# Optimization experiments

Hardware: AMD Instinct MI355X
Metric: run time of the kernel (lower is better)

Reference implementation:

```python
import jax, jax.numpy as jnp
import numpy as np

EPS = 1e-08  # matches torch default eps in both F.normalize and PairwiseDistance


def setup_inputs() -> dict:
    key = jax.random.key(0)
    x = jax.random.normal(key, (8192, 1024), dtype=jnp.float32)
    return {"x": x}


def reference(x) -> jnp.ndarray:
    B = x.shape[0]
    # F.normalize(x, p=2, dim=-1, eps=EPS): x / max(||x||_2, eps)
    norms = jnp.linalg.norm(x, axis=-1, keepdims=True)
    xn = x / jnp.maximum(norms, EPS)
    # cosine similarity matrix [B, B]
    cos_sim = xn @ xn.T
    # fill_diagonal_(-2): exclude self from nearest-neighbor search
    idx = jnp.arange(B)
    cos_sim = cos_sim.at[idx, idx].set(-2.0)
    nn_idx = jnp.argmax(cos_sim, axis=1)  # [B] int
    # torch PairwiseDistance(p=2, eps=EPS): ||x1 - x2 + eps||_2
    diff = xn - xn[nn_idx] + EPS
    nn_dist = jnp.sqrt(jnp.sum(diff * diff, axis=-1))  # [B]
    loss = -jnp.mean(jnp.log(nn_dist + EPS))
    return loss
```

## Files before the change

### kernel.cpp

```cpp
#include <hip/hip_runtime.h>
#include <hip/hip_bf16.h>
#include <math.h>

#define NB 8192
#define ND 1024
#define KEPS 1e-8f
#define SLOTS 128
#define NTILE 32
#define NWG 528
#define NKT 16

typedef __attribute__((ext_vector_type(8))) __bf16 bf16x8;
typedef __attribute__((ext_vector_type(4))) float f32x4;

__device__ __forceinline__ unsigned int fmono(float f) {
    unsigned int b = __float_as_uint(f);
    return b ^ ((b & 0x80000000u) ? 0xFFFFFFFFu : 0x80000000u);
}
__device__ __forceinline__ unsigned short f2bf(float f) {
    union { float f; unsigned int u; } a;
    a.f = f;
    unsigned int lsb = (a.u >> 16) & 1u;
    a.u += 0x7fffu + lsb;
    return (unsigned short)(a.u >> 16);
}
__device__ __forceinline__ void gload_lds16(const void* g, void* l) {
    __builtin_amdgcn_global_load_lds(
        (const __attribute__((address_space(1))) unsigned int*)g,
        (__attribute__((address_space(3))) unsigned int*)l, 16, 0, 0);
}
__device__ __forceinline__ unsigned long long packmax(float mx, int mc) {
    return ((unsigned long long)fmono(mx) << 32) |
           (unsigned long long)(~(unsigned int)mc);
}

__global__ __launch_bounds__(256) void normalize_k(const float* __restrict__ x,
                                                   unsigned short* __restrict__ xnb) {
    int row = blockIdx.x * 4 + (threadIdx.x >> 6);
    int l = threadIdx.x & 63;
    const float4* xr = (const float4*)(x + (size_t)row * ND);
    float4 v[4];
    float ss = 0.f;
#pragma unroll
    for (int q = 0; q < 4; ++q) {
        v[q] = xr[q * 64 + l];
        ss += v[q].x * v[q].x + v[q].y * v[q].y + v[q].z * v[q].z + v[q].w * v[q].w;
    }
#pragma unroll
    for (int off = 1; off < 64; off <<= 1) ss += __shfl_xor(ss, off, 64);
    float scale = 1.0f / fmaxf(sqrtf(ss), KEPS);
    ushort4* o = (ushort4*)(xnb + (size_t)row * ND);
#pragma unroll
    for (int q = 0; q < 4; ++q) {
        ushort4 u;
        u.x = f2bf(v[q].x * scale);
        u.y = f2bf(v[q].y * scale);
        u.z = f2bf(v[q].z * scale);
        u.w = f2bf(v[q].w * scale);
        o[q * 64 + l] = u;
    }
}

#define FENCE_BARRIER() do { asm volatile("" ::: "memory"); \
    __builtin_amdgcn_s_barrier(); asm volatile("" ::: "memory"); } while (0)
#define WAIT_VM6() asm volatile("s_waitcnt vmcnt(6)" ::: "memory")
#define WAIT_VM0() asm volatile("s_waitcnt vmcnt(0)" ::: "memory")

#define STAGE(H, DB) do { \
    gload_lds16(sp[H][0], ldsb + (DB) + (H) * 16384 + wv * 1024); \
    gload_lds16(sp[H][1], ldsb + (DB) + (H) * 16384 + 8192 + wv * 1024); \
    sp[H][0] += 128; sp[H][1] += 128; } while (0)

#define LOAD_A(CB, MQ) do { \
    const char* Ab_ = ldsb + (CB) + ((MQ) * 2 + wM) * 8192 + rowOff; \
    _Pragma("unroll") for (int mi = 0; mi < 4; ++mi) { \
        af[mi][0] = *(const bf16x8*)(Ab_ + mi * 2048 + ks0); \
        af[mi][1] = *(const bf16x8*)(Ab_ + mi * 2048 + ks1); } } while (0)

#define LOAD_B(CB, BANK, NQ) do { \
    const char* Bb_ = ldsb + (CB) + 32768 + (NQ) * 16384 + wN * 4096 + rowOff; \
    _Pragma("unroll") for (int ni = 0; ni < 2; ++ni) { \
        BANK[ni][0] = *(const bf16x8*)(Bb_ + ni * 2048 + ks0); \
        BANK[ni][1] = *(const bf16x8*)(Bb_ + ni * 2048 + ks1); } } while (0)

#define MFMAQ(MH, NH, BANK) do { \
    __builtin_amdgcn_s_setprio(1); \
    _Pragma("unroll") for (int mi = 0; mi < 4; ++mi) \
    _Pragma("unroll") for (int ni = 0; ni < 2; ++ni) { \
        acc[(MH) * 4 + mi][(NH) * 2 + ni] = __builtin_amdgcn_mfma_f32_16x16x32_bf16( \
            af[mi][0], BANK[ni][0], acc[(MH) * 4 + mi][(NH) * 2 + ni], 0, 0, 0); \
        acc[(MH) * 4 + mi][(NH) * 2 + ni] = __builtin_amdgcn_mfma_f32_16x16x32_bf16( \
            af[mi][1], BANK[ni][1], acc[(MH) * 4 + mi][(NH) * 2 + ni], 0, 0, 0); } \
    __builtin_amdgcn_s_setprio(0); } while (0)

#define KTILE(CB, DB, S1, S2, FINAL) do { \
    bf16x8 af[4][2], b0[2][2], b1[2][2]; \
    LOAD_A(CB, 0); LOAD_B(CB, b0, 0); \
    if (S1) STAGE(1, DB); \
    FENCE_BARRIER(); MFMAQ(0, 0, b0); FENCE_BARRIER(); \
    LOAD_B(CB, b1, 1); \
    if (S2) STAGE(0, CB); \
    FENCE_BARRIER(); MFMAQ(0, 1, b1); FENCE_BARRIER(); \
    LOAD_A(CB, 1); \
    if (S2) STAGE(2, CB); \
    FENCE_BARRIER(); MFMAQ(1, 1, b1); FENCE_BARRIER(); \
    if (S2) STAGE(3, CB); \
    MFMAQ(1, 0, b0); \
    if (FINAL) { WAIT_VM0(); } else { WAIT_VM6(); } \
    FENCE_BARRIER(); } while (0)

#define KTILE_LAST(CB) do { \
    bf16x8 af[4][2], b0[2][2], b1[2][2]; \
    LOAD_A(CB, 0); LOAD_B(CB, b0, 0); \
    FENCE_BARRIER(); MFMAQ(0, 0, b0); FENCE_BARRIER(); \
    LOAD_B(CB, b1, 1); \
    FENCE_BARRIER(); MFMAQ(0, 1, b1); FENCE_BARRIER(); \
    LOAD_A(CB, 1); \
    FENCE_BARRIER(); MFMAQ(1, 1, b1); FENCE_BARRIER(); \
    MFMAQ(1, 0, b0); } while (0)

__global__ __launch_bounds__(512, 2) void argmax_gemm(const unsigned short* __restrict__ xnb,
                                                      unsigned long long* __restrict__ partial) {
    extern __shared__ char ldsb[];

    int wg = (int)blockIdx.x;
    int tile = (wg & 7) * (NWG / 8) + (wg >> 3);
    int by = 0, tr = tile;
    while (tr >= NTILE - by) { tr -= NTILE - by; ++by; }
    const int bx = by + tr;

    const int rowBase = by * 256, colBase = bx * 256;
    const int tid = (int)threadIdx.x;
    const int wv = tid >> 6;
    const int l = tid & 63;
    const int wM = wv >> 2;
    const int wN = wv & 3;

    const int rowOff = (l & 15) * 128;
    const int ks0 = (((l >> 4) * 16)) ^ ((l & 7) << 4);
    const int ks1 = (64 | ((l >> 4) * 16)) ^ ((l & 7) << 4);

    const int scol = (((l & 7) ^ (l >> 3)) << 4);
    const char* xb = (const char*)xnb;
    const char* sp[4][2];
#pragma unroll
    for (int q = 0; q < 2; ++q) {
        int R = (q * 8 + wv) * 8 + (l >> 3);
        int arow = (R >> 6) * 128 + (R & 63);
        int bcol = (R >> 5) * 64 + (R & 31);
        sp[0][q] = xb + (size_t)(rowBase + arow) * 2048 + scol;
        sp[1][q] = xb + (size_t)(rowBase + arow + 64) * 2048 + scol;
        sp[2][q] = xb + (size_t)(colBase + bcol) * 2048 + scol;
        sp[3][q] = xb + (size_t)(colBase + bcol + 32) * 2048 + scol;
    }

    STAGE(0, 0); STAGE(2, 0); STAGE(3, 0); STAGE(1, 0);
    STAGE(0, 65536); STAGE(2, 65536); STAGE(3, 65536);

    f32x4 acc[8][4];
#pragma unroll
    for (int m = 0; m < 8; ++m)
#pragma unroll
        for (int n = 0; n < 4; ++n) acc[m][n] = f32x4{0.f, 0.f, 0.f, 0.f};

    WAIT_VM6();
    FENCE_BARRIER();

    for (int c = 0; c < 12; c += 2) {
        KTILE(0, 65536, true, true, false);
        KTILE(65536, 0, true, true, false);
    }
    KTILE(0, 65536, true, true, false);
    KTILE(65536, 0, true, true, false);
    KTILE(0, 65536, true, false, true);
    KTILE_LAST(65536);

#pragma unroll
    for (int m = 0; m < 8; ++m) {
#pragma unroll
        for (int r = 0; r < 4; ++r) {
            int gi = rowBase + wM * 128 + m * 16 + (l >> 4) * 4 + r;
            float mx = -3.0f;
            int mc = 0x7FFFFFFF;
#pragma unroll
            for (int n = 0; n < 4; ++n) {
                int gj = colBase + wN * 64 + n * 16 + (l & 15);
                float v = (gi == gj) ? -2.0f : acc[m][n][r];
                if (v > mx) { mx = v; mc = gj; }
            }
#pragma unroll
            for (int off = 1; off < 16; off <<= 1) {
                float omx = __shfl_xor(mx, off, 64);
                int omc = __shfl_xor(mc, off, 64);
                if (omx > mx || (omx == mx && omc < mc)) { mx = omx; mc = omc; }
            }
            if ((l & 15) == 0)
                partial[(size_t)gi * SLOTS + (2 * by + (bx - by) * 4 + wN)] = packmax(mx, mc);
        }
    }
    if (bx > by) {
#pragma unroll
        for (int n = 0; n < 4; ++n) {
            int gj = colBase + wN * 64 + n * 16 + (l & 15);
            float mx = -3.0f;
            int mc = 0x7FFFFFFF;
#pragma unroll
            for (int m = 0; m < 8; ++m) {
#pragma unroll
                for (int r = 0; r < 4; ++r) {
                    int gi = rowBase + wM * 128 + m * 16 + (l >> 4) * 4 + r;
                    float v = (gi == gj) ? -2.0f : acc[m][n][r];
                    if (v > mx) { mx = v; mc = gi; }
                }
            }
#pragma unroll
            for (int off = 16; off < 64; off <<= 1) {
                float omx = __shfl_xor(mx, off, 64);
                int omc = __shfl_xor(mc, off, 64);
                if (omx > mx || (omx == mx && omc < mc)) { mx = omx; mc = omc; }
            }
            if ((l >> 4) == 0)
                partial[(size_t)gj * SLOTS + (2 * by + wM)] = packmax(mx, mc);
        }
    }
}

__global__ __launch_bounds__(256) void dist_k(const float* __restrict__ x,
                                              const unsigned long long* __restrict__ partial,
                                              float* __restrict__ rowloss) {
    int i = blockIdx.x * 4 + (threadIdx.x >> 6);
    int l = threadIdx.x & 63;
    int nv = SLOTS - 2 * (i >> 8);
    unsigned long long p = 0ull;
    if (l < nv) p = partial[(size_t)i * SLOTS + l];
    if (l + 64 < nv) {
        unsigned long long o = partial[(size_t)i * SLOTS + l + 64];
        if (o > p) p = o;
    }
#pragma unroll
    for (int off = 1; off < 64; off <<= 1) {
        unsigned long long o = __shfl_xor(p, off, 64);
        if (o > p) p = o;
    }
    int j = (int)(~(unsigned int)(p & 0xFFFFFFFFull));

    const float4* xi = (const float4*)(x + (size_t)i * ND);
    const float4* xj = (const float4*)(x + (size_t)j * ND);
    float4 a[4], b[4];
    float sa = 0.f, sb = 0.f;
#pragma unroll
    for (int q = 0; q < 4; ++q) {
        a[q] = xi[q * 64 + l];
        b[q] = xj[q * 64 + l];
        sa += a[q].x * a[q].x + a[q].y * a[q].y + a[q].z * a[q].z + a[q].w * a[q].w;
        sb += b[q].x * b[q].x + b[q].y * b[q].y + b[q].z * b[q].z + b[q].w * b[q].w;
    }
#pragma unroll
    for (int off = 1; off < 64; off <<= 1) {
        sa += __shfl_xor(sa, off, 64);
        sb += __shfl_xor(sb, off, 64);
    }
    float ia = 1.0f / fmaxf(sqrtf(sa), KEPS);
    float ib = 1.0f / fmaxf(sqrtf(sb), KEPS);
    float ss = 0.f;
#pragma unroll
    for (int q = 0; q < 4; ++q) {
        float dx = a[q].x * ia - b[q].x * ib + KEPS;
        float dy = a[q].y * ia - b[q].y * ib + KEPS;
        float dz = a[q].z * ia - b[q].z * ib + KEPS;
        float dw = a[q].w * ia - b[q].w * ib + KEPS;
        ss += dx * dx + dy * dy + dz * dz + dw * dw;
    }
#pragma unroll
    for (int off = 1; off < 64; off <<= 1) ss += __shfl_xor(ss, off, 64);
    if (l == 0) rowloss[i] = -logf(sqrtf(ss) + KEPS);
}

__global__ __launch_bounds__(1024) void reduce_k(const float* __restrict__ rowloss,
                                                 float* __restrict__ out) {
    int t = threadIdx.x;
    float s = 0.0f;
#pragma unroll
    for (int k = 0; k < 8; ++k) s += rowloss[t + k * 1024];
#pragma unroll
    for (int off = 32; off > 0; off >>= 1) s += __shfl_down(s, off, 64);
    __shared__ float sred[16];
    if ((t & 63) == 0) sred[t >> 6] = s;
    __syncthreads();
    if (t == 0) {
        float tot = 0.0f;
        for (int k = 0; k < 16; ++k) tot += sred[k];
        out[0] = tot / (float)NB;
    }
}

extern "C" void kernel_launch(void* const* d_in, const int* in_sizes, int n_in,
                              void* d_out, int out_size, void* d_ws, size_t ws_size,
                              hipStream_t stream) {
    const float* x = (const float*)d_in[0];
    float* out = (float*)d_out;

    char* ws = (char*)d_ws;
    unsigned short* xnb = (unsigned short*)ws;
    unsigned long long* partial =
        (unsigned long long*)(ws + (size_t)NB * ND * 2);
    float* rowloss = (float*)(ws + (size_t)NB * ND * 2 + (size_t)NB * SLOTS * 8);

    (void)hipFuncSetAttribute((const void*)argmax_gemm,
                              hipFuncAttributeMaxDynamicSharedMemorySize, 131072);

    normalize_k<<<NB / 4, 256, 0, stream>>>(x, xnb);
    argmax_gemm<<<NWG, 512, 131072, stream>>>(xnb, partial);
    dist_k<<<NB / 4, 256, 0, stream>>>(x, partial, rowloss);
    reduce_k<<<1, 1024, 0, stream>>>(rowloss, out);
}
```

Baseline: 222.4 us.

## Shrink argmax GEMM tiles to 128x128 with simpler double-buffered K loop

Replaces the 256x256 tile, 512-thread GEMM with a 128x128 tile, 256-thread kernel using 32KB static LDS, a 32-wide K step and a plain double-buffered stage/compute loop. The aim is higher occupancy and simpler scheduling. The cost is lower arithmetic intensity per tile, more global/L2 traffic over four times as many workgroups, and loss of the interleaved LDS-read/MFMA schedule with priority hints. The partial-slot indexing changes so every row now fills all 128 slots, which lets dist_k drop its bounds checks.

```diff
diff --git a/kernel.cpp b/kernel.cpp
--- a/kernel.cpp
+++ b/kernel.cpp
@@ -6,9 +6,9 @@
 #define ND 1024
 #define KEPS 1e-8f
 #define SLOTS 128
-#define NTILE 32
-#define NWG 528
-#define NKT 16
+#define NTIL 64
+#define NWG 2080
+#define NKT 32
 
 typedef __attribute__((ext_vector_type(8))) __bf16 bf16x8;
 typedef __attribute__((ext_vector_type(4))) float f32x4;
@@ -63,129 +63,81 @@
 
 #define FENCE_BARRIER() do { asm volatile("" ::: "memory"); \
     __builtin_amdgcn_s_barrier(); asm volatile("" ::: "memory"); } while (0)
-#define WAIT_VM6() asm volatile("s_waitcnt vmcnt(6)" ::: "memory")
+#define WAIT_VM4() asm volatile("s_waitcnt vmcnt(4)" ::: "memory")
 #define WAIT_VM0() asm volatile("s_waitcnt vmcnt(0)" ::: "memory")
 
-#define STAGE(H, DB) do { \
-    gload_lds16(sp[H][0], ldsb + (DB) + (H) * 16384 + wv * 1024); \
-    gload_lds16(sp[H][1], ldsb + (DB) + (H) * 16384 + 8192 + wv * 1024); \
-    sp[H][0] += 128; sp[H][1] += 128; } while (0)
-
-#define LOAD_A(CB, MQ) do { \
-    const char* Ab_ = ldsb + (CB) + ((MQ) * 2 + wM) * 8192 + rowOff; \
-    _Pragma("unroll") for (int mi = 0; mi < 4; ++mi) { \
-        af[mi][0] = *(const bf16x8*)(Ab_ + mi * 2048 + ks0); \
-        af[mi][1] = *(const bf16x8*)(Ab_ + mi * 2048 + ks1); } } while (0)
-
-#define LOAD_B(CB, BANK, NQ) do { \
-    const char* Bb_ = ldsb + (CB) + 32768 + (NQ) * 16384 + wN * 4096 + rowOff; \
-    _Pragma("unroll") for (int ni = 0; ni < 2; ++ni) { \
-        BANK[ni][0] = *(const bf16x8*)(Bb_ + ni * 2048 + ks0); \
-        BANK[ni][1] = *(const bf16x8*)(Bb_ + ni * 2048 + ks1); } } while (0)
-
-#define MFMAQ(MH, NH, BANK) do { \
-    __builtin_amdgcn_s_setprio(1); \
+#define STAGEALL(DB) do { \
+    gload_lds16(spA0, ldsb + (DB) + (wv * 2 + 0) * 1024); \
+    gload_lds16(spA1, ldsb + (DB) + (wv * 2 + 1) * 1024); \
+    gload_lds16(spB0, ldsb + (DB) + 8192 + (wv * 2 + 0) * 1024); \
+    gload_lds16(spB1, ldsb + (DB) + 8192 + (wv * 2 + 1) * 1024); \
+    spA0 += 64; spA1 += 64; spB0 += 64; spB1 += 64; } while (0)
+
+#define KT(CB, DB, PF) do { \
+    if (PF) { STAGEALL(DB); WAIT_VM4(); } else { WAIT_VM0(); } \
+    FENCE_BARRIER(); \
+    bf16x8 af[4], bf[4]; \
     _Pragma("unroll") for (int mi = 0; mi < 4; ++mi) \
-    _Pragma("unroll") for (int ni = 0; ni < 2; ++ni) { \
-        acc[(MH) * 4 + mi][(NH) * 2 + ni] = __builtin_amdgcn_mfma_f32_16x16x32_bf16( \
-            af[mi][0], BANK[ni][0], acc[(MH) * 4 + mi][(NH) * 2 + ni], 0, 0, 0); \
-        acc[(MH) * 4 + mi][(NH) * 2 + ni] = __builtin_amdgcn_mfma_f32_16x16x32_bf16( \
-            af[mi][1], BANK[ni][1], acc[(MH) * 4 + mi][(NH) * 2 + ni], 0, 0, 0); } \
-    __builtin_amdgcn_s_setprio(0); } while (0)
-
-#define KTILE(CB, DB, S1, S2, FINAL) do { \
-    bf16x8 af[4][2], b0[2][2], b1[2][2]; \
-    LOAD_A(CB, 0); LOAD_B(CB, b0, 0); \
-    if (S1) STAGE(1, DB); \
-    FENCE_BARRIER(); MFMAQ(0, 0, b0); FENCE_BARRIER(); \
-    LOAD_B(CB, b1, 1); \
-    if (S2) STAGE(0, CB); \
-    FENCE_BARRIER(); MFMAQ(0, 1, b1); FENCE_BARRIER(); \
-    LOAD_A(CB, 1); \
-    if (S2) STAGE(2, CB); \
-    FENCE_BARRIER(); MFMAQ(1, 1, b1); FENCE_BARRIER(); \
-    if (S2) STAGE(3, CB); \
-    MFMAQ(1, 0, b0); \
-    if (FINAL) { WAIT_VM0(); } else { WAIT_VM6(); } \
+        af[mi] = *(const bf16x8*)(ldsb + (CB) + wM * 4096 + mi * 1024 + rowks); \
+    _Pragma("unroll") for (int ni = 0; ni < 4; ++ni) \
+        bf[ni] = *(const bf16x8*)(ldsb + (CB) + 8192 + wN * 4096 + ni * 1024 + rowks); \
+    _Pragma("unroll") for (int mi = 0; mi < 4; ++mi) \
+    _Pragma("unroll") for (int ni = 0; ni < 4; ++ni) \
+        acc[mi][ni] = __builtin_amdgcn_mfma_f32_16x16x32_bf16(af[mi], bf[ni], acc[mi][ni], 0, 0, 0); \
     FENCE_BARRIER(); } while (0)
 
-#define KTILE_LAST(CB) do { \
-    bf16x8 af[4][2], b0[2][2], b1[2][2]; \
-    LOAD_A(CB, 0); LOAD_B(CB, b0, 0); \
-    FENCE_BARRIER(); MFMAQ(0, 0, b0); FENCE_BARRIER(); \
-    LOAD_B(CB, b1, 1); \
-    FENCE_BARRIER(); MFMAQ(0, 1, b1); FENCE_BARRIER(); \
-    LOAD_A(CB, 1); \
-    FENCE_BARRIER(); MFMAQ(1, 1, b1); FENCE_BARRIER(); \
-    MFMAQ(1, 0, b0); } while (0)
-
-__global__ __launch_bounds__(512, 2) void argmax_gemm(const unsigned short* __restrict__ xnb,
+__global__ __launch_bounds__(256, 4) void argmax_gemm(const unsigned short* __restrict__ xnb,
                                                       unsigned long long* __restrict__ partial) {
-    extern __shared__ char ldsb[];
+    __shared__ char ldsb[32768];
 
     int wg = (int)blockIdx.x;
     int tile = (wg & 7) * (NWG / 8) + (wg >> 3);
     int by = 0, tr = tile;
-    while (tr >= NTILE - by) { tr -= NTILE - by; ++by; }
+    while (tr >= NTIL - by) { tr -= NTIL - by; ++by; }
     const int bx = by + tr;
 
-    const int rowBase = by * 256, colBase = bx * 256;
+    const int rowBase = by * 128, colBase = bx * 128;
     const int tid = (int)threadIdx.x;
     const int wv = tid >> 6;
     const int l = tid & 63;
-    const int wM = wv >> 2;
-    const int wN = wv & 3;
-
-    const int rowOff = (l & 15) * 128;
-    const int ks0 = (((l >> 4) * 16)) ^ ((l & 7) << 4);
-    const int ks1 = (64 | ((l >> 4) * 16)) ^ ((l & 7) << 4);
-
-    const int scol = (((l & 7) ^ (l >> 3)) << 4);
+    const int wM = wv >> 1;
+    const int wN = wv & 1;
+
+    const int rowks = (l & 15) * 64 + (((l >> 4) * 16) ^ (((l >> 1) & 3) << 4));
+
+    const int scol = (((l & 3) ^ ((l >> 3) & 3)) << 4);
     const char* xb = (const char*)xnb;
-    const char* sp[4][2];
-#pragma unroll
-    for (int q = 0; q < 2; ++q) {
-        int R = (q * 8 + wv) * 8 + (l >> 3);
-        int arow = (R >> 6) * 128 + (R & 63);
-        int bcol = (R >> 5) * 64 + (R & 31);
-        sp[0][q] = xb + (size_t)(rowBase + arow) * 2048 + scol;
-        sp[1][q] = xb + (size_t)(rowBase + arow + 64) * 2048 + scol;
-        sp[2][q] = xb + (size_t)(colBase + bcol) * 2048 + scol;
-        sp[3][q] = xb + (size_t)(colBase + bcol + 32) * 2048 + scol;
-    }
-
-    STAGE(0, 0); STAGE(2, 0); STAGE(3, 0); STAGE(1, 0);
-    STAGE(0, 65536); STAGE(2, 65536); STAGE(3, 65536);
-
-    f32x4 acc[8][4];
-#pragma unroll
-    for (int m = 0; m < 8; ++m)
+    const int r0 = (wv * 2 + 0) * 16 + (l >> 2);
+    const int r1 = (wv * 2 + 1) * 16 + (l >> 2);
+    const char* spA0 = xb + (size_t)(rowBase + r0) * 2048 + scol;
+    const char* spA1 = xb + (size_t)(rowBase + r1) * 2048 + scol;
+    const char* spB0 = xb + (size_t)(colBase + r0) * 2048 + scol;
+    const char* spB1 = xb + (size_t)(colBase + r1) * 2048 + scol;
+
+    f32x4 acc[4][4];
+#pragma unroll
+    for (int m = 0; m < 4; ++m)
 #pragma unroll
         for (int n = 0; n < 4; ++n) acc[m][n] = f32x4{0.f, 0.f, 0.f, 0.f};
 
-    WAIT_VM6();
-    FENCE_BARRIER();
-
-    for (int c = 0; c < 12; c += 2) {
-        KTILE(0, 65536, true, true, false);
-        KTILE(65536, 0, true, true, false);
-    }
-    KTILE(0, 65536, true, true, false);
-    KTILE(65536, 0, true, true, false);
-    KTILE(0, 65536, true, false, true);
-    KTILE_LAST(65536);
-
-#pragma unroll
-    for (int m = 0; m < 8; ++m) {
+    STAGEALL(0);
+
+    for (int c = 0; c < NKT; c += 2) {
+        KT(0, 16384, c + 1 < NKT);
+        KT(16384, 0, c + 2 < NKT);
+    }
+
+#pragma unroll
+    for (int mi = 0; mi < 4; ++mi) {
 #pragma unroll
         for (int r = 0; r < 4; ++r) {
-            int gi = rowBase + wM * 128 + m * 16 + (l >> 4) * 4 + r;
+            int gi = rowBase + wM * 64 + mi * 16 + (l >> 4) * 4 + r;
             float mx = -3.0f;
             int mc = 0x7FFFFFFF;
 #pragma unroll
-            for (int n = 0; n < 4; ++n) {
-                int gj = colBase + wN * 64 + n * 16 + (l & 15);
-                float v = (gi == gj) ? -2.0f : acc[m][n][r];
+            for (int ni = 0; ni < 4; ++ni) {
+                int gj = colBase + wN * 64 + ni * 16 + (l & 15);
+                float v = (gi == gj) ? -2.0f : acc[mi][ni][r];
                 if (v > mx) { mx = v; mc = gj; }
             }
 #pragma unroll
@@ -195,21 +147,21 @@
                 if (omx > mx || (omx == mx && omc < mc)) { mx = omx; mc = omc; }
             }
             if ((l & 15) == 0)
-                partial[(size_t)gi * SLOTS + (2 * by + (bx - by) * 4 + wN)] = packmax(mx, mc);
+                partial[(size_t)gi * SLOTS + (bx - by) * 2 + wN] = packmax(mx, mc);
         }
     }
     if (bx > by) {
 #pragma unroll
-        for (int n = 0; n < 4; ++n) {
-            int gj = colBase + wN * 64 + n * 16 + (l & 15);
+        for (int ni = 0; ni < 4; ++ni) {
+            int gj = colBase + wN * 64 + ni * 16 + (l & 15);
             float mx = -3.0f;
             int mc = 0x7FFFFFFF;
 #pragma unroll
-            for (int m = 0; m < 8; ++m) {
+            for (int mi = 0; mi < 4; ++mi) {
 #pragma unroll
                 for (int r = 0; r < 4; ++r) {
-                    int gi = rowBase + wM * 128 + m * 16 + (l >> 4) * 4 + r;
-                    float v = (gi == gj) ? -2.0f : acc[m][n][r];
+                    int gi = rowBase + wM * 64 + mi * 16 + (l >> 4) * 4 + r;
+                    float v = (gi == gj) ? -2.0f : acc[mi][ni][r];
                     if (v > mx) { mx = v; mc = gi; }
                 }
             }
@@ -220,7 +172,7 @@
                 if (omx > mx || (omx == mx && omc < mc)) { mx = omx; mc = omc; }
             }
             if ((l >> 4) == 0)
-                partial[(size_t)gj * SLOTS + (2 * by + wM)] = packmax(mx, mc);
+                partial[(size_t)gj * SLOTS + (NTIL - bx) * 2 + by * 2 + wM] = packmax(mx, mc);
         }
     }
 }
@@ -230,10 +182,8 @@
                                               float* __restrict__ rowloss) {
     int i = blockIdx.x * 4 + (threadIdx.x >> 6);
     int l = threadIdx.x & 63;
-    int nv = SLOTS - 2 * (i >> 8);
-    unsigned long long p = 0ull;
-    if (l < nv) p = partial[(size_t)i * SLOTS + l];
-    if (l + 64 < nv) {
+    unsigned long long p = partial[(size_t)i * SLOTS + l];
+    {
         unsigned long long o = partial[(size_t)i * SLOTS + l + 64];
         if (o > p) p = o;
     }
@@ -306,11 +256,8 @@
         (unsigned long long*)(ws + (size_t)NB * ND * 2);
     float* rowloss = (float*)(ws + (size_t)NB * ND * 2 + (size_t)NB * SLOTS * 8);
 
-    (void)hipFuncSetAttribute((const void*)argmax_gemm,
-                              hipFuncAttributeMaxDynamicSharedMemorySize, 131072);
-
     normalize_k<<<NB / 4, 256, 0, stream>>>(x, xnb);
-    argmax_gemm<<<NWG, 512, 131072, stream>>>(xnb, partial);
+    argmax_gemm<<<NWG, 256, 0, stream>>>(xnb, partial);
     dist_k<<<NB / 4, 256, 0, stream>>>(x, partial, rowloss);
     reduce_k<<<1, 1024, 0, stream>>>(rowloss, out);
 }
```

Result: faster. 184.7 us (-17.0%).
